# Performance work log

Measured on AMD Instinct MI355X. Metric: run time of the kernel, lower is better.

The kernel has to match this reference:

```python
import jax, jax.numpy as jnp
import numpy as np

D_MODEL = 1024
N_HEADS = 16
B, T = 4, 2048


def setup_inputs() -> dict:
    key = jax.random.key(0)
    ks = jax.random.split(key, 5)
    s_in = 1.0 / np.sqrt(D_MODEL)
    x = jax.random.normal(ks[0], (B, T, D_MODEL), dtype=jnp.float32)
    W_qkv = jax.random.uniform(ks[1], (D_MODEL, 3 * D_MODEL), jnp.float32, -s_in, s_in)
    b_qkv = jax.random.uniform(ks[2], (3 * D_MODEL,), jnp.float32, -s_in, s_in)
    W_proj = jax.random.uniform(ks[3], (D_MODEL, D_MODEL), jnp.float32, -s_in, s_in)
    b_proj = jax.random.uniform(ks[4], (D_MODEL,), jnp.float32, -s_in, s_in)
    return {"x": x, "W_qkv": W_qkv, "b_qkv": b_qkv, "W_proj": W_proj, "b_proj": b_proj}


def reference(x, W_qkv, b_qkv, W_proj, b_proj):
    b, t, c = x.shape
    hd = c // N_HEADS  # head dim
    qkv = x @ W_qkv + b_qkv                      # [B,T,3C]
    q, k, v = jnp.split(qkv, 3, axis=2)
    # [B,T,C] -> [B,H,T,hd]
    def heads(z):
        return z.reshape(b, t, N_HEADS, hd).transpose(0, 2, 1, 3)
    q, k, v = heads(q), heads(k), heads(v)
    att = jnp.einsum('bhqd,bhkd->bhqk', q, k) * (1.0 / np.sqrt(hd))
    causal = jnp.tril(jnp.ones((t, t), dtype=bool))
    att = jnp.where(causal, att, -jnp.inf)
    att = jax.nn.softmax(att, axis=-1)
    y = jnp.einsum('bhqk,bhkd->bhqd', att, v)    # [B,H,T,hd]
    y = y.transpose(0, 2, 1, 3).reshape(b, t, c)
    return y @ W_proj + b_proj
```

## Files before the change

kernel.cpp:

```cpp
#include <hip/hip_runtime.h>
#include <hip/hip_bf16.h>

typedef __attribute__((ext_vector_type(4))) float f32x4;
typedef __attribute__((ext_vector_type(8))) short s16x8;
typedef __attribute__((ext_vector_type(4))) short s16x4;

#define D_MODEL 1024
#define NH 16
#define HD 64
#define BB 4
#define TT 2048
#define MROWS (BB * TT)
#define QSCALE 0.18033688011112042f

#define MFMA16(a, b, c) __builtin_amdgcn_mfma_f32_16x16x32_bf16(a, b, c, 0, 0, 0)

#if __has_builtin(__builtin_amdgcn_mfma_f32_16x16x16_bf16)
#define PVMFMA(a, b, c) __builtin_amdgcn_mfma_f32_16x16x16_bf16(a, b, c, 0, 0, 0)
#elif __has_builtin(__builtin_amdgcn_mfma_f32_16x16x16bf16_1k)
#define PVMFMA(a, b, c) __builtin_amdgcn_mfma_f32_16x16x16bf16_1k(a, b, c, 0, 0, 0)
#else
static __device__ __forceinline__ f32x4 pv_mfma_asm(s16x4 a, s16x4 b, f32x4 c) {
  asm volatile("v_mfma_f32_16x16x16_bf16 %0, %1, %2, %0\n\ts_nop 7\n\ts_nop 7"
               : "+v"(c)
               : "v"(a), "v"(b));
  return c;
}
#define PVMFMA(a, b, c) pv_mfma_asm(a, b, c)
#endif

#define GLL16(g, l)                                                                   \
  __builtin_amdgcn_global_load_lds((const __attribute__((address_space(1))) void*)(g), \
                                   (__attribute__((address_space(3))) void*)(l), 16, 0, 0)

static __device__ __forceinline__ unsigned short f2bf(float f) {
  unsigned int u = __float_as_uint(f);
  u += 0x7fff + ((u >> 16) & 1);
  return (unsigned short)(u >> 16);
}

__global__ void k_convert(const float* __restrict__ src, short* __restrict__ dst, int n4) {
  int i = blockIdx.x * blockDim.x + threadIdx.x;
  if (i >= n4) return;
  f32x4 v = reinterpret_cast<const f32x4*>(src)[i];
  s16x4 o;
#pragma unroll
  for (int r = 0; r < 4; r++) o[r] = (short)f2bf(v[r]);
  reinterpret_cast<s16x4*>(dst)[i] = o;
}

__global__ void k_transpose(const float* __restrict__ src, short* __restrict__ dst, int K, int N) {
  __shared__ float tile[32][33];
  int n0 = blockIdx.x * 32, k0 = blockIdx.y * 32;
  int tx = threadIdx.x, ty = threadIdx.y;
#pragma unroll
  for (int i = 0; i < 4; i++) tile[ty + i * 8][tx] = src[(size_t)(k0 + ty + i * 8) * N + n0 + tx];
  __syncthreads();
#pragma unroll
  for (int i = 0; i < 4; i++)
    dst[(size_t)(n0 + ty + i * 8) * K + k0 + tx] = (short)f2bf(tile[tx][ty + i * 8]);
}

__global__ __launch_bounds__(512, 2) void k_gemm_qkv(
    const short* __restrict__ A, const short* __restrict__ Bt, const float* __restrict__ bias,
    short* __restrict__ outQ, short* __restrict__ outK, short* __restrict__ outV) {
  const int K = D_MODEL;
  __shared__ __align__(16) short lds_a[2][256 * 64];
  __shared__ __align__(16) short lds_b[2][128 * 64];
  const int tid = threadIdx.x;
  const int m0 = blockIdx.y * 256, n0 = blockIdx.x * 128;
  const int w = tid >> 6, lane = tid & 63;
  const int wm = (w >> 1) * 64, wn = (w & 1) * 64;
  const int lr = lane & 15, lg = lane >> 4;
  const int srow = lane >> 3;
  const int scol = ((lane & 7) ^ srow) * 8;
  const int r7 = lr & 7;

  const short* aGb = A + (size_t)(m0 + w * 32 + srow) * K + scol;
  const short* bGb = Bt + (size_t)(n0 + w * 16 + srow) * K + scol;

#define QSTAGE(bi, kt)                                                  \
  {                                                                     \
    GLL16(aGb + (kt), &lds_a[bi][(w * 32) * 64]);                       \
    GLL16(aGb + (size_t)8 * K + (kt), &lds_a[bi][(w * 32 + 8) * 64]);   \
    GLL16(aGb + (size_t)16 * K + (kt), &lds_a[bi][(w * 32 + 16) * 64]); \
    GLL16(aGb + (size_t)24 * K + (kt), &lds_a[bi][(w * 32 + 24) * 64]); \
    GLL16(bGb + (kt), &lds_b[bi][(w * 16) * 64]);                       \
    GLL16(bGb + (size_t)8 * K + (kt), &lds_b[bi][(w * 16 + 8) * 64]);   \
  }

  f32x4 acc[4][4] = {};
  const int NT = K / 64;
  QSTAGE(0, 0);
  __syncthreads();
  for (int t = 0; t < NT; ++t) {
    const int cur = t & 1;
    if (t + 1 < NT) QSTAGE(cur ^ 1, (t + 1) * 64);
#pragma unroll
    for (int ks = 0; ks < 2; ks++) {
      s16x8 af[4], bfg[4];
#pragma unroll
      for (int i = 0; i < 4; i++)
        af[i] = *(const s16x8*)&lds_a[cur][(wm + i * 16 + lr) * 64 + ((ks * 4 + lg) ^ r7) * 8];
#pragma unroll
      for (int j = 0; j < 4; j++)
        bfg[j] = *(const s16x8*)&lds_b[cur][(wn + j * 16 + lr) * 64 + ((ks * 4 + lg) ^ r7) * 8];
#pragma unroll
      for (int i = 0; i < 4; i++) {
#pragma unroll
        for (int j = 0; j < 4; j++) acc[i][j] = MFMA16(af[i], bfg[j], acc[i][j]);
      }
    }
    __syncthreads();
  }
#undef QSTAGE

#pragma unroll
  for (int j = 0; j < 4; j++) {
    const int ng = n0 + wn + j * 16 + lr;
    const float bv = bias[ng];
#pragma unroll
    for (int i = 0; i < 4; i++) {
      const int mg = m0 + wm + i * 16 + 4 * lg;
      const int sec = ng >> 10, c = ng & 1023, h = c >> 6, d = c & 63;
      const int b = mg >> 11, t = mg & 2047;
      const int bh = b * NH + h;
      if (sec == 2) {
        s16x4 pk;
#pragma unroll
        for (int r = 0; r < 4; r++) pk[r] = (short)f2bf(acc[i][j][r] + bv);
        *(s16x4*)&outV[((size_t)bh * HD + d) * TT + t] = pk;
      } else {
        short* dst = (sec == 0) ? outQ : outK;
        const float sc = (sec == 0) ? QSCALE : 1.0f;
#pragma unroll
        for (int r = 0; r < 4; r++)
          dst[((size_t)bh * TT + t + r) * HD + d] = (short)f2bf((acc[i][j][r] + bv) * sc);
      }
    }
  }
}

__global__ __launch_bounds__(512, 2) void k_gemm_proj(
    const short* __restrict__ A, const short* __restrict__ Bt, const float* __restrict__ bias,
    float* __restrict__ outF) {
  const int K = D_MODEL, N = D_MODEL;
  __shared__ __align__(16) short lds_a[2][256 * 64];
  __shared__ __align__(16) short lds_b[2][128 * 64];
  const int tid = threadIdx.x;
  const int m0 = blockIdx.y * 256, n0 = blockIdx.x * 128;
  const int w = tid >> 6, lane = tid & 63;
  const int wm = (w >> 1) * 64, wn = (w & 1) * 64;
  const int lr = lane & 15, lg = lane >> 4;
  const int srow = lane >> 3;
  const int scol = ((lane & 7) ^ srow) * 8;
  const int r7 = lr & 7;

  const short* aGb = A + (size_t)(m0 + w * 32 + srow) * K + scol;
  const short* bGb = Bt + (size_t)(n0 + w * 16 + srow) * K + scol;

#define PSTAGE(bi, kt)                                                  \
  {                                                                     \
    GLL16(aGb + (kt), &lds_a[bi][(w * 32) * 64]);                       \
    GLL16(aGb + (size_t)8 * K + (kt), &lds_a[bi][(w * 32 + 8) * 64]);   \
    GLL16(aGb + (size_t)16 * K + (kt), &lds_a[bi][(w * 32 + 16) * 64]); \
    GLL16(aGb + (size_t)24 * K + (kt), &lds_a[bi][(w * 32 + 24) * 64]); \
    GLL16(bGb + (kt), &lds_b[bi][(w * 16) * 64]);                       \
    GLL16(bGb + (size_t)8 * K + (kt), &lds_b[bi][(w * 16 + 8) * 64]);   \
  }

  f32x4 acc[4][4] = {};
  const int NT = K / 64;
  PSTAGE(0, 0);
  __syncthreads();
  for (int t = 0; t < NT; ++t) {
    const int cur = t & 1;
    if (t + 1 < NT) PSTAGE(cur ^ 1, (t + 1) * 64);
#pragma unroll
    for (int ks = 0; ks < 2; ks++) {
      s16x8 af[4], bfg[4];
#pragma unroll
      for (int i = 0; i < 4; i++)
        af[i] = *(const s16x8*)&lds_a[cur][(wm + i * 16 + lr) * 64 + ((ks * 4 + lg) ^ r7) * 8];
#pragma unroll
      for (int j = 0; j < 4; j++)
        bfg[j] = *(const s16x8*)&lds_b[cur][(wn + j * 16 + lr) * 64 + ((ks * 4 + lg) ^ r7) * 8];
#pragma unroll
      for (int i = 0; i < 4; i++) {
#pragma unroll
        for (int j = 0; j < 4; j++) acc[i][j] = MFMA16(af[i], bfg[j], acc[i][j]);
      }
    }
    __syncthreads();
  }
#undef PSTAGE

#pragma unroll
  for (int j = 0; j < 4; j++) {
    const int ng = n0 + wn + j * 16 + lr;
    const float bv = bias[ng];
#pragma unroll
    for (int i = 0; i < 4; i++) {
      const int mg = m0 + wm + i * 16 + 4 * lg;
#pragma unroll
      for (int r = 0; r < 4; r++) outF[(size_t)(mg + r) * N + ng] = acc[i][j][r] + bv;
    }
  }
}

__global__ __launch_bounds__(256, 3) void k_attn(const short* __restrict__ Q,
                                                 const short* __restrict__ Kb,
                                                 const short* __restrict__ Vt,
                                                 short* __restrict__ Y) {
  __shared__ __align__(16) short kls[2][64 * 64];
  __shared__ __align__(16) short vls[2][64 * 64];
  const int tid = threadIdx.x, w = tid >> 6, lane = tid & 63;
  const int lr = lane & 15, lg = lane >> 4;
  const int p = blockIdx.x + 8 * blockIdx.y;
  const int xcd = p & 7, idx = p >> 3;
  const int bh = xcd * 8 + (idx >> 3);
  const int xq = idx & 7;
  const int b = bh >> 4, h = bh & 15;
  const short* Qh = Q + (size_t)bh * TT * HD;
  const short* Kh = Kb + (size_t)bh * TT * HD;
  const short* Vh = Vt + (size_t)bh * HD * TT;
  const int srow = lane >> 3;
  const int scol = ((lane & 7) ^ srow) * 8;
  const int r7 = lr & 7;
  const s16x4 vone = {(short)0x3F80, (short)0x3F80, (short)0x3F80, (short)0x3F80};

#define STAGE(bi, kv0)                                                   \
  {                                                                      \
    const short* ks_ = Kh + (size_t)((kv0) + w * 16 + srow) * HD + scol; \
    GLL16(ks_, &kls[bi][(w * 16) * 64]);                                 \
    GLL16(ks_ + 8 * HD, &kls[bi][(w * 16 + 8) * 64]);                    \
    const short* vs_ = Vh + (size_t)(w * 16 + srow) * TT + (kv0) + scol; \
    GLL16(vs_, &vls[bi][(w * 16) * 64]);                                 \
    GLL16(vs_ + 8 * TT, &vls[bi][(w * 16 + 8) * 64]);                    \
  }

#pragma unroll
  for (int ph = 0; ph < 2; ph++) {
    const int panel = ph ? (15 - xq) : xq;
    const int q0w = panel * 128 + w * 32;
    s16x8 qf[2][2];
#pragma unroll
    for (int jq = 0; jq < 2; jq++)
#pragma unroll
      for (int kc = 0; kc < 2; kc++)
        qf[jq][kc] = *(const s16x8*)&Qh[(q0w + jq * 16 + lr) * HD + kc * 32 + lg * 8];

    f32x4 sacc[2] = {};
    f32x4 oacc[2][4] = {};

    const int nt = 2 * panel + 2;
    STAGE(0, 0);
    __syncthreads();
    for (int t = 0; t < nt; ++t) {
      const int cur = t & 1;
      if (t + 1 < nt) STAGE(cur ^ 1, (t + 1) * 64);
      const int kv0 = t * 64;
      s16x8 kf[4][2];
#pragma unroll
      for (int jk = 0; jk < 4; jk++)
#pragma unroll
        for (int kc = 0; kc < 2; kc++)
          kf[jk][kc] = *(const s16x8*)&kls[cur][(jk * 16 + lr) * 64 + ((kc * 4 + lg) ^ r7) * 8];
      s16x4 pf16[2][4];
#pragma unroll
      for (int jq = 0; jq < 2; jq++) {
        f32x4 s[4] = {};
#pragma unroll
        for (int kc = 0; kc < 2; kc++)
#pragma unroll
          for (int jk = 0; jk < 4; jk++) s[jk] = MFMA16(kf[jk][kc], qf[jq][kc], s[jk]);
        const bool diag = (kv0 + 63 > q0w + jq * 16);
        const int qg = q0w + jq * 16 + lr;
#pragma unroll
        for (int jk = 0; jk < 4; jk++) {
#pragma unroll
          for (int r = 0; r < 4; r++) {
            float pp = exp2f(s[jk][r]);
            if (diag) {
              const int kvg = kv0 + jk * 16 + 4 * lg + r;
              pp = (kvg <= qg) ? pp : 0.f;
            }
            pf16[jq][jk][r] = (short)((__float_as_uint(pp) + 0x8000) >> 16);
          }
        }
      }
#pragma unroll
      for (int jk = 0; jk < 4; jk++) {
        s16x4 vreg[4];
#pragma unroll
        for (int jd = 0; jd < 4; jd++)
          vreg[jd] = *(const s16x4*)&vls[cur][(jd * 16 + lr) * 64 +
                                              ((2 * jk + (lg >> 1)) ^ r7) * 8 + (lg & 1) * 4];
#pragma unroll
        for (int jq = 0; jq < 2; jq++) {
          sacc[jq] = PVMFMA(vone, pf16[jq][jk], sacc[jq]);
#pragma unroll
          for (int jd = 0; jd < 4; jd++)
            oacc[jq][jd] = PVMFMA(vreg[jd], pf16[jq][jk], oacc[jq][jd]);
        }
      }
      __syncthreads();
    }
#pragma unroll
    for (int jq = 0; jq < 2; jq++) {
      const float inv = 1.0f / sacc[jq][0];
      const int trow = q0w + jq * 16 + lr;
#pragma unroll
      for (int jd = 0; jd < 4; jd++) {
        s16x4 pk;
#pragma unroll
        for (int r = 0; r < 4; r++) pk[r] = (short)f2bf(oacc[jq][jd][r] * inv);
        *(s16x4*)&Y[((size_t)(b * TT + trow)) * D_MODEL + h * HD + jd * 16 + 4 * lg] = pk;
      }
    }
  }
#undef STAGE
}

extern "C" void kernel_launch(void* const* d_in, const int* in_sizes, int n_in,
                              void* d_out, int out_size, void* d_ws, size_t ws_size,
                              hipStream_t stream) {
  const float* x = (const float*)d_in[0];
  const float* Wqkv = (const float*)d_in[1];
  const float* bqkv = (const float*)d_in[2];
  const float* Wproj = (const float*)d_in[3];
  const float* bproj = (const float*)d_in[4];
  float* out = (float*)d_out;

  char* ws = (char*)d_ws;
  short* Xb = (short*)ws;
  short* Wqkvt = (short*)(ws + (16u << 20));
  short* Wprojt = (short*)(ws + (22u << 20));
  short* Qb = (short*)(ws + (24u << 20));
  short* Kb = (short*)(ws + (40u << 20));
  short* Vtb = (short*)(ws + (56u << 20));
  short* Yb = Xb;

  k_convert<<<dim3(MROWS * D_MODEL / 4 / 256), 256, 0, stream>>>(x, Xb, MROWS * D_MODEL / 4);
  k_transpose<<<dim3(3 * D_MODEL / 32, D_MODEL / 32), dim3(32, 8), 0, stream>>>(
      Wqkv, Wqkvt, D_MODEL, 3 * D_MODEL);
  k_transpose<<<dim3(D_MODEL / 32, D_MODEL / 32), dim3(32, 8), 0, stream>>>(
      Wproj, Wprojt, D_MODEL, D_MODEL);
  k_gemm_qkv<<<dim3(3 * D_MODEL / 128, MROWS / 256), 512, 0, stream>>>(
      Xb, Wqkvt, bqkv, Qb, Kb, Vtb);
  k_attn<<<dim3(8, BB * NH), 256, 0, stream>>>(Qb, Kb, Vtb, Yb);
  k_gemm_proj<<<dim3(D_MODEL / 128, MROWS / 256), 512, 0, stream>>>(
      Yb, Wprojt, bproj, out);
}
```

Before: 307.6 us.

## Retile QKV GEMM to 256x192 and halve attention query panel size

```diff
diff --git a/kernel.cpp b/kernel.cpp
--- a/kernel.cpp
+++ b/kernel.cpp
@@ -66,18 +66,18 @@
     short* __restrict__ outQ, short* __restrict__ outK, short* __restrict__ outV) {
   const int K = D_MODEL;
   __shared__ __align__(16) short lds_a[2][256 * 64];
-  __shared__ __align__(16) short lds_b[2][128 * 64];
+  __shared__ __align__(16) short lds_b[2][192 * 64];
   const int tid = threadIdx.x;
-  const int m0 = blockIdx.y * 256, n0 = blockIdx.x * 128;
+  const int m0 = blockIdx.y * 256, n0 = blockIdx.x * 192;
   const int w = tid >> 6, lane = tid & 63;
-  const int wm = (w >> 1) * 64, wn = (w & 1) * 64;
+  const int wm = (w >> 2) * 128, wn = (w & 3) * 48;
   const int lr = lane & 15, lg = lane >> 4;
   const int srow = lane >> 3;
   const int scol = ((lane & 7) ^ srow) * 8;
   const int r7 = lr & 7;
 
   const short* aGb = A + (size_t)(m0 + w * 32 + srow) * K + scol;
-  const short* bGb = Bt + (size_t)(n0 + w * 16 + srow) * K + scol;
+  const short* bGb = Bt + (size_t)(n0 + w * 24 + srow) * K + scol;
 
 #define QSTAGE(bi, kt)                                                  \
   {                                                                     \
@@ -85,11 +85,12 @@
     GLL16(aGb + (size_t)8 * K + (kt), &lds_a[bi][(w * 32 + 8) * 64]);   \
     GLL16(aGb + (size_t)16 * K + (kt), &lds_a[bi][(w * 32 + 16) * 64]); \
     GLL16(aGb + (size_t)24 * K + (kt), &lds_a[bi][(w * 32 + 24) * 64]); \
-    GLL16(bGb + (kt), &lds_b[bi][(w * 16) * 64]);                       \
-    GLL16(bGb + (size_t)8 * K + (kt), &lds_b[bi][(w * 16 + 8) * 64]);   \
-  }
-
-  f32x4 acc[4][4] = {};
+    GLL16(bGb + (kt), &lds_b[bi][(w * 24) * 64]);                       \
+    GLL16(bGb + (size_t)8 * K + (kt), &lds_b[bi][(w * 24 + 8) * 64]);   \
+    GLL16(bGb + (size_t)16 * K + (kt), &lds_b[bi][(w * 24 + 16) * 64]); \
+  }
+
+  f32x4 acc[8][3] = {};
   const int NT = K / 64;
   QSTAGE(0, 0);
   __syncthreads();
@@ -98,17 +99,17 @@
     if (t + 1 < NT) QSTAGE(cur ^ 1, (t + 1) * 64);
 #pragma unroll
     for (int ks = 0; ks < 2; ks++) {
-      s16x8 af[4], bfg[4];
-#pragma unroll
-      for (int i = 0; i < 4; i++)
+      s16x8 af[8], bfg[3];
+#pragma unroll
+      for (int i = 0; i < 8; i++)
         af[i] = *(const s16x8*)&lds_a[cur][(wm + i * 16 + lr) * 64 + ((ks * 4 + lg) ^ r7) * 8];
 #pragma unroll
-      for (int j = 0; j < 4; j++)
+      for (int j = 0; j < 3; j++)
         bfg[j] = *(const s16x8*)&lds_b[cur][(wn + j * 16 + lr) * 64 + ((ks * 4 + lg) ^ r7) * 8];
 #pragma unroll
-      for (int i = 0; i < 4; i++) {
-#pragma unroll
-        for (int j = 0; j < 4; j++) acc[i][j] = MFMA16(af[i], bfg[j], acc[i][j]);
+      for (int i = 0; i < 8; i++) {
+#pragma unroll
+        for (int j = 0; j < 3; j++) acc[i][j] = MFMA16(af[i], bfg[j], acc[i][j]);
       }
     }
     __syncthreads();
@@ -116,11 +117,11 @@
 #undef QSTAGE
 
 #pragma unroll
-  for (int j = 0; j < 4; j++) {
+  for (int j = 0; j < 3; j++) {
     const int ng = n0 + wn + j * 16 + lr;
     const float bv = bias[ng];
 #pragma unroll
-    for (int i = 0; i < 4; i++) {
+    for (int i = 0; i < 8; i++) {
       const int mg = m0 + wm + i * 16 + 4 * lg;
       const int sec = ng >> 10, c = ng & 1023, h = c >> 6, d = c & 63;
       const int b = mg >> 11, t = mg & 2047;
@@ -208,7 +209,7 @@
   }
 }
 
-__global__ __launch_bounds__(256, 3) void k_attn(const short* __restrict__ Q,
+__global__ __launch_bounds__(256, 4) void k_attn(const short* __restrict__ Q,
                                                  const short* __restrict__ Kb,
                                                  const short* __restrict__ Vt,
                                                  short* __restrict__ Y) {
@@ -216,10 +217,10 @@
   __shared__ __align__(16) short vls[2][64 * 64];
   const int tid = threadIdx.x, w = tid >> 6, lane = tid & 63;
   const int lr = lane & 15, lg = lane >> 4;
-  const int p = blockIdx.x + 8 * blockIdx.y;
+  const int p = blockIdx.x + 16 * blockIdx.y;
   const int xcd = p & 7, idx = p >> 3;
-  const int bh = xcd * 8 + (idx >> 3);
-  const int xq = idx & 7;
+  const int bh = xcd * 8 + (idx >> 4);
+  const int xq = idx & 15;
   const int b = bh >> 4, h = bh & 15;
   const short* Qh = Q + (size_t)bh * TT * HD;
   const short* Kh = Kb + (size_t)bh * TT * HD;
@@ -241,19 +242,17 @@
 
 #pragma unroll
   for (int ph = 0; ph < 2; ph++) {
-    const int panel = ph ? (15 - xq) : xq;
-    const int q0w = panel * 128 + w * 32;
-    s16x8 qf[2][2];
-#pragma unroll
-    for (int jq = 0; jq < 2; jq++)
-#pragma unroll
-      for (int kc = 0; kc < 2; kc++)
-        qf[jq][kc] = *(const s16x8*)&Qh[(q0w + jq * 16 + lr) * HD + kc * 32 + lg * 8];
-
-    f32x4 sacc[2] = {};
-    f32x4 oacc[2][4] = {};
-
-    const int nt = 2 * panel + 2;
+    const int panel = ph ? (31 - xq) : xq;
+    const int q0w = panel * 64 + w * 16;
+    s16x8 qf[2];
+#pragma unroll
+    for (int kc = 0; kc < 2; kc++)
+      qf[kc] = *(const s16x8*)&Qh[(q0w + lr) * HD + kc * 32 + lg * 8];
+
+    f32x4 sacc = {0.f, 0.f, 0.f, 0.f};
+    f32x4 oacc[4] = {};
+
+    const int nt = panel + 1;
     STAGE(0, 0);
     __syncthreads();
     for (int t = 0; t < nt; ++t) {
@@ -266,27 +265,25 @@
 #pragma unroll
         for (int kc = 0; kc < 2; kc++)
           kf[jk][kc] = *(const s16x8*)&kls[cur][(jk * 16 + lr) * 64 + ((kc * 4 + lg) ^ r7) * 8];
-      s16x4 pf16[2][4];
-#pragma unroll
-      for (int jq = 0; jq < 2; jq++) {
-        f32x4 s[4] = {};
-#pragma unroll
-        for (int kc = 0; kc < 2; kc++)
-#pragma unroll
-          for (int jk = 0; jk < 4; jk++) s[jk] = MFMA16(kf[jk][kc], qf[jq][kc], s[jk]);
-        const bool diag = (kv0 + 63 > q0w + jq * 16);
-        const int qg = q0w + jq * 16 + lr;
-#pragma unroll
-        for (int jk = 0; jk < 4; jk++) {
-#pragma unroll
-          for (int r = 0; r < 4; r++) {
-            float pp = exp2f(s[jk][r]);
-            if (diag) {
-              const int kvg = kv0 + jk * 16 + 4 * lg + r;
-              pp = (kvg <= qg) ? pp : 0.f;
-            }
-            pf16[jq][jk][r] = (short)((__float_as_uint(pp) + 0x8000) >> 16);
+      f32x4 s[4] = {};
+#pragma unroll
+      for (int kc = 0; kc < 2; kc++)
+#pragma unroll
+        for (int jk = 0; jk < 4; jk++) s[jk] = MFMA16(kf[jk][kc], qf[kc], s[jk]);
+
+      const bool diag = (kv0 + 63 > q0w);
+      const int qg = q0w + lr;
+      s16x4 pf16[4];
+#pragma unroll
+      for (int jk = 0; jk < 4; jk++) {
+#pragma unroll
+        for (int r = 0; r < 4; r++) {
+          float pp = exp2f(s[jk][r]);
+          if (diag) {
+            const int kvg = kv0 + jk * 16 + 4 * lg + r;
+            pp = (kvg <= qg) ? pp : 0.f;
           }
+          pf16[jk][r] = (short)((__float_as_uint(pp) + 0x8000) >> 16);
         }
       }
 #pragma unroll
@@ -296,27 +293,20 @@
         for (int jd = 0; jd < 4; jd++)
           vreg[jd] = *(const s16x4*)&vls[cur][(jd * 16 + lr) * 64 +
                                               ((2 * jk + (lg >> 1)) ^ r7) * 8 + (lg & 1) * 4];
-#pragma unroll
-        for (int jq = 0; jq < 2; jq++) {
-          sacc[jq] = PVMFMA(vone, pf16[jq][jk], sacc[jq]);
-#pragma unroll
-          for (int jd = 0; jd < 4; jd++)
-            oacc[jq][jd] = PVMFMA(vreg[jd], pf16[jq][jk], oacc[jq][jd]);
-        }
+        sacc = PVMFMA(vone, pf16[jk], sacc);
+#pragma unroll
+        for (int jd = 0; jd < 4; jd++) oacc[jd] = PVMFMA(vreg[jd], pf16[jk], oacc[jd]);
       }
       __syncthreads();
     }
-#pragma unroll
-    for (int jq = 0; jq < 2; jq++) {
-      const float inv = 1.0f / sacc[jq][0];
-      const int trow = q0w + jq * 16 + lr;
-#pragma unroll
-      for (int jd = 0; jd < 4; jd++) {
-        s16x4 pk;
-#pragma unroll
-        for (int r = 0; r < 4; r++) pk[r] = (short)f2bf(oacc[jq][jd][r] * inv);
-        *(s16x4*)&Y[((size_t)(b * TT + trow)) * D_MODEL + h * HD + jd * 16 + 4 * lg] = pk;
-      }
+    const float inv = 1.0f / sacc[0];
+    const int trow = q0w + lr;
+#pragma unroll
+    for (int jd = 0; jd < 4; jd++) {
+      s16x4 pk;
+#pragma unroll
+      for (int r = 0; r < 4; r++) pk[r] = (short)f2bf(oacc[jd][r] * inv);
+      *(s16x4*)&Y[((size_t)(b * TT + trow)) * D_MODEL + h * HD + jd * 16 + 4 * lg] = pk;
     }
   }
 #undef STAGE
@@ -346,9 +336,9 @@
       Wqkv, Wqkvt, D_MODEL, 3 * D_MODEL);
   k_transpose<<<dim3(D_MODEL / 32, D_MODEL / 32), dim3(32, 8), 0, stream>>>(
       Wproj, Wprojt, D_MODEL, D_MODEL);
-  k_gemm_qkv<<<dim3(3 * D_MODEL / 128, MROWS / 256), 512, 0, stream>>>(
+  k_gemm_qkv<<<dim3(3 * D_MODEL / 192, MROWS / 256), 512, 0, stream>>>(
       Xb, Wqkvt, bqkv, Qb, Kb, Vtb);
-  k_attn<<<dim3(8, BB * NH), 256, 0, stream>>>(Qb, Kb, Vtb, Yb);
+  k_attn<<<dim3(16, BB * NH), 256, 0, stream>>>(Qb, Kb, Vtb, Yb);
   k_gemm_proj<<<dim3(D_MODEL / 128, MROWS / 256), 512, 0, stream>>>(
       Yb, Wprojt, bproj, out);
 }
```

Result: faster. 290.9 us (-5.5%).
